# Kernel optimization log

Measured on AMD Instinct MI355X. Metric: run time of the kernel, lower is better.

## Reference

```python
import jax, jax.numpy as jnp
import numpy as np

N = 100000   # nodes
E = 1600000  # edges
F = 128      # n_feat
HID = 64     # n_hid
L = 4        # n_layer
C = 40       # n_class
TEMP = 0.1   # summarize temperature


def setup_inputs() -> dict:
    key = jax.random.key(0)
    ks = jax.random.split(key, 10)
    x = jax.random.normal(ks[0], (N, F), dtype=jnp.float32)
    edge_index = jax.random.randint(ks[1], (2, E), 0, N, dtype=jnp.int64)
    s_in = 1.0 / np.sqrt(F)
    s_h = 1.0 / np.sqrt(HID)
    W0 = jax.random.normal(ks[2], (F, HID), dtype=jnp.float32) * s_in
    b0 = jnp.zeros((HID,), dtype=jnp.float32)
    Ws = jax.random.normal(ks[3], (L - 1, HID, HID), dtype=jnp.float32) * s_h
    bs = jnp.zeros((L - 1, HID), dtype=jnp.float32)
    Wq = jax.random.normal(ks[4], (HID, HID), dtype=jnp.float32) * s_h
    Wk = jax.random.normal(ks[5], (HID, HID), dtype=jnp.float32) * s_h
    Wout = jax.random.normal(ks[6], (HID, C), dtype=jnp.float32) * s_h
    bout = jnp.zeros((C,), dtype=jnp.float32)
    return {"x": x, "edge_index": edge_index, "W0": W0, "b0": b0,
            "Ws": Ws, "bs": bs, "Wq": Wq, "Wk": Wk, "Wout": Wout, "bout": bout}


def reference(x, edge_index, W0, b0, Ws, bs, Wq, Wk, Wout, bout):
    # --- GCN normalization with self-loops (symmetric D^-1/2 (A+I) D^-1/2) ---
    loop = jnp.arange(N, dtype=edge_index.dtype)
    src = jnp.concatenate([edge_index[0], loop])  # [E+N]
    dst = jnp.concatenate([edge_index[1], loop])
    deg = jax.ops.segment_sum(jnp.ones_like(dst, dtype=x.dtype), dst, num_segments=N)
    dinv = jnp.where(deg > 0, jax.lax.rsqrt(deg), 0.0)
    enorm = dinv[src] * dinv[dst]  # [E+N]

    def propagate(h):
        # gather -> scale -> scatter-add (sparse matvec)
        msg = h[src] * enorm[:, None]
        return jax.ops.segment_sum(msg, dst, num_segments=N)

    # --- twin-branch stacked GCN convs (x_ starts as detached copy; eval mode => no dropout) ---
    h, h_ = x, x
    hs, hs_ = [], []
    for l in range(L):
        W = W0 if l == 0 else Ws[l - 1]
        b = b0 if l == 0 else bs[l - 1]
        h = jax.nn.relu(propagate(h @ W) + b)
        h_ = jax.nn.relu(propagate(h_ @ W) + b)
        hs.append(h)
        hs_.append(h_)

    Hm = jnp.stack(hs)    # [L, N, HID]
    Hm_ = jnp.stack(hs_)  # [L, N, HID]

    # --- Summarize: per-node attention over layer scales; query from twin branch ---
    q = jnp.einsum('lnd,de->lne', Hm_, Wq)
    k = jnp.einsum('lnd,de->lne', Hm, Wk)
    scores = jnp.sum(q * k, axis=-1) / TEMP      # [L, N]
    att = jax.nn.softmax(scores, axis=0)         # softmax over layers
    hsum = jnp.einsum('ln,lnd->nd', att, Hm)     # [N, HID]

    return hsum @ Wout + bout                    # [N, C]
```

## Files before the change

### kernel.cpp

```cpp
#include <hip/hip_runtime.h>
#include <hip/hip_bf16.h>
#include <math.h>

#define NN 100000
#define EE 1600000
#define FF 128
#define HH 64
#define CC 40

constexpr int SCAN_B = 1024;
constexpr int NB = (NN + SCAN_B - 1) / SCAN_B;

typedef unsigned long long u64;
typedef float f32x4 __attribute__((ext_vector_type(4)));

constexpr int NBUK = 125;
constexpr int RNB = 800;
constexpr int BCAP3 = 13800;
constexpr int NE_BLK = 4000;
constexpr int ABLK = EE / NE_BLK;

__global__ void k_init(int* __restrict__ bcnt) {
    int i = threadIdx.x;
    if (i < NBUK) bcnt[i] = 0;
}

__global__ __launch_bounds__(256) void k_bucket(const int* __restrict__ ei, int* __restrict__ bcnt,
                                                u64* __restrict__ bpr) {
    __shared__ int lcnt[NBUK], lbase[NBUK], loff[NBUK];
    const int t = threadIdx.x;
    for (int k = t; k < NBUK; k += 256) { lcnt[k] = 0; loff[k] = 0; }
    __syncthreads();
    const int e0 = blockIdx.x * NE_BLK;
    int es[16], ed[16];
#pragma unroll
    for (int k = 0; k < 16; ++k) {
        int idx = t + k * 256;
        if (idx < NE_BLK) {
            es[k] = ei[e0 + idx];
            ed[k] = ei[EE + e0 + idx];
            atomicAdd(&lcnt[ed[k] / RNB], 1);
        }
    }
    __syncthreads();
    for (int k = t; k < NBUK; k += 256) lbase[k] = atomicAdd(&bcnt[k], lcnt[k]);
    __syncthreads();
#pragma unroll
    for (int k = 0; k < 16; ++k) {
        int idx = t + k * 256;
        if (idx < NE_BLK) {
            int b = ed[k] / RNB;
            int pos = lbase[b] + atomicAdd(&loff[b], 1);
            if (pos < BCAP3) {
                bpr[(size_t)b * BCAP3 + pos] = (u64)(unsigned)es[k] | ((u64)(unsigned)ed[k] << 32);
            }
        }
    }
}

__global__ __launch_bounds__(512) void k_count3(const u64* __restrict__ bpr, const int* __restrict__ bcnt,
                                                int* __restrict__ deg) {
    __shared__ int h[RNB];
    const int t = threadIdx.x, b = blockIdx.x;
    for (int k = t; k < RNB; k += 512) h[k] = 0;
    __syncthreads();
    const int cnt = min(bcnt[b], BCAP3);
    const u64* __restrict__ pp = bpr + (size_t)b * BCAP3;
    const int lo = b * RNB;
    for (int i = t; i < cnt; i += 512) atomicAdd(&h[(int)(pp[i] >> 32) - lo], 1);
    __syncthreads();
    for (int k = t; k < RNB; k += 512) deg[lo + k] = h[k] + 1;
}

__global__ void k_dinv(const int* __restrict__ deg, float* __restrict__ dinv) {
    int i = blockIdx.x * 256 + threadIdx.x;
    if (i < NN) dinv[i] = rsqrtf((float)deg[i]);
}

__global__ void k_scanA(const int* __restrict__ deg, int* __restrict__ excl, int* __restrict__ bsum) {
    __shared__ int s[SCAN_B];
    int t = threadIdx.x;
    int g = blockIdx.x * SCAN_B + t;
    int v = (g < NN) ? deg[g] : 0;
    s[t] = v;
    __syncthreads();
    for (int o = 1; o < SCAN_B; o <<= 1) {
        int u = (t >= o) ? s[t - o] : 0;
        __syncthreads();
        s[t] += u;
        __syncthreads();
    }
    if (g < NN) excl[g] = s[t] - v;
    if (t == SCAN_B - 1) bsum[blockIdx.x] = s[t];
}

__global__ void k_scanB(int* __restrict__ bsum) {
    __shared__ int s[128];
    int t = threadIdx.x;
    int v = (t < NB) ? bsum[t] : 0;
    s[t] = v;
    __syncthreads();
    for (int o = 1; o < 128; o <<= 1) {
        int u = (t >= o) ? s[t - o] : 0;
        __syncthreads();
        s[t] += u;
        __syncthreads();
    }
    if (t < NB) bsum[t] = s[t] - v;
}

__global__ void k_scanC(int* __restrict__ rp, const int* __restrict__ bsum) {
    int t = threadIdx.x;
    int g = blockIdx.x * SCAN_B + t;
    if (g < NN) rp[g] = rp[g] + bsum[blockIdx.x];
    if (g == 0) rp[NN] = EE + NN;
}

__global__ __launch_bounds__(512) void k_fill3(const u64* __restrict__ bpr, const int* __restrict__ bcnt,
                                               const int* __restrict__ rp, int* __restrict__ cs) {
    __shared__ int lcur[RNB];
    __shared__ int lbuf[RNB + BCAP3];
    const int t = threadIdx.x, b = blockIdx.x;
    const int lo = b * RNB;
    const int rpl = rp[lo];
    for (int k = t; k < RNB; k += 512) lcur[k] = rp[lo + k] - rpl;
    __syncthreads();
    const int cnt = min(bcnt[b], BCAP3);
    const u64* __restrict__ pp = bpr + (size_t)b * BCAP3;
    for (int i = t; i < cnt; i += 512) {
        u64 u = pp[i];
        int pos = atomicAdd(&lcur[(int)(u >> 32) - lo], 1);
        lbuf[pos] = (int)(unsigned)u;
    }
    __syncthreads();
    for (int k = t; k < RNB; k += 512) {
        int pos = atomicAdd(&lcur[k], 1);
        lbuf[pos] = lo + k;
    }
    __syncthreads();
    const int total = rp[lo + RNB] - rpl;
    for (int i = t; i < total; i += 512) __builtin_nontemporal_store(lbuf[i], cs + rpl + i);
}

template <int K>
__global__ __launch_bounds__(256) void k_gemm(const float* __restrict__ A, const float* __restrict__ W,
                                              const float* __restrict__ dinv, float* __restrict__ Z,
                                              int nrows) {
    constexpr int S = 68;
    __shared__ float wl[64 * 64];
    __shared__ float hl[64 * S];
    const int t = threadIdx.x;
    const int r0 = blockIdx.x * 64;
    const int rg = t >> 4, cg = t & 15;
    float acc[4][4] = {};

    for (int kb = 0; kb < K; kb += 64) {
        {
            const float4* Wv = (const float4*)(W + kb * 64);
            for (int i = t; i < 1024; i += 256) ((float4*)wl)[i] = Wv[i];
        }
        for (int i = t; i < 1024; i += 256) {
            int row = i >> 4, d4 = i & 15;
            float4 v = {0.f, 0.f, 0.f, 0.f};
            if (r0 + row < nrows) v = *(const float4*)(A + (size_t)(r0 + row) * K + kb + d4 * 4);
            *(float4*)(hl + row * S + d4 * 4) = v;
        }
        __syncthreads();
#pragma unroll 8
        for (int d = 0; d < 64; ++d) {
            float4 w4 = *(const float4*)(wl + d * 64 + cg * 4);
#pragma unroll
            for (int i = 0; i < 4; i++) {
                float h = hl[(rg * 4 + i) * S + d];
                acc[i][0] = fmaf(h, w4.x, acc[i][0]);
                acc[i][1] = fmaf(h, w4.y, acc[i][1]);
                acc[i][2] = fmaf(h, w4.z, acc[i][2]);
                acc[i][3] = fmaf(h, w4.w, acc[i][3]);
            }
        }
        __syncthreads();
    }
#pragma unroll
    for (int i = 0; i < 4; i++) {
        int row = r0 + rg * 4 + i;
        if (row < nrows) {
            float dv = dinv[row];
            float4 o = {acc[i][0] * dv, acc[i][1] * dv, acc[i][2] * dv, acc[i][3] * dv};
            *(float4*)(Z + (size_t)row * 64 + cg * 4) = o;
        }
    }
}

__global__ __launch_bounds__(256) void k_prepM(const float* __restrict__ Wq, const float* __restrict__ Wk,
                                               float* __restrict__ M) {
    __shared__ float wk[64 * 65];
    __shared__ float wq[4 * 64];
    const int t = threadIdx.x;
    for (int i = t; i < 1024; i += 256) {
        int r = i >> 4, c4 = i & 15;
        float4 v = ((const float4*)Wk)[i];
        wk[r * 65 + c4 * 4 + 0] = v.x;
        wk[r * 65 + c4 * 4 + 1] = v.y;
        wk[r * 65 + c4 * 4 + 2] = v.z;
        wk[r * 65 + c4 * 4 + 3] = v.w;
    }
    const int rbase = blockIdx.x * 4;
    wq[t] = Wq[rbase * 64 + t];
    __syncthreads();
    const int rr = t >> 6;
    const int c = t & 63;
    float acc = 0.f;
#pragma unroll 8
    for (int e = 0; e < 64; ++e) acc = fmaf(wq[rr * 64 + e], wk[c * 65 + e], acc);
    M[(rbase + rr) * 64 + c] = acc;
}

__global__ __launch_bounds__(256) void k_prop(const float* __restrict__ z, const int* __restrict__ rp,
                                              const int* __restrict__ cs, const float* __restrict__ dinv,
                                              const float* __restrict__ bias, float* __restrict__ out) {
    const int lane = threadIdx.x & 63;
    const int g = lane >> 4;
    const int l4 = lane & 15;
    const int n = blockIdx.x * 16 + (threadIdx.x >> 6) * 4 + g;
    const int beg = rp[n], end = rp[n + 1];
    float4 a0 = {0, 0, 0, 0}, a1 = {0, 0, 0, 0}, a2 = {0, 0, 0, 0}, a3 = {0, 0, 0, 0};
    int i = beg;
    for (; i + 8 <= end; i += 8) {
        int c0 = __builtin_nontemporal_load(cs + i);
        int c1 = __builtin_nontemporal_load(cs + i + 1);
        int c2 = __builtin_nontemporal_load(cs + i + 2);
        int c3 = __builtin_nontemporal_load(cs + i + 3);
        int c4 = __builtin_nontemporal_load(cs + i + 4);
        int c5 = __builtin_nontemporal_load(cs + i + 5);
        int c6 = __builtin_nontemporal_load(cs + i + 6);
        int c7 = __builtin_nontemporal_load(cs + i + 7);
        float4 z0 = *(const float4*)(z + (size_t)(unsigned)c0 * 64 + l4 * 4);
        float4 z1 = *(const float4*)(z + (size_t)(unsigned)c1 * 64 + l4 * 4);
        float4 z2 = *(const float4*)(z + (size_t)(unsigned)c2 * 64 + l4 * 4);
        float4 z3 = *(const float4*)(z + (size_t)(unsigned)c3 * 64 + l4 * 4);
        float4 z4 = *(const float4*)(z + (size_t)(unsigned)c4 * 64 + l4 * 4);
        float4 z5 = *(const float4*)(z + (size_t)(unsigned)c5 * 64 + l4 * 4);
        float4 z6 = *(const float4*)(z + (size_t)(unsigned)c6 * 64 + l4 * 4);
        float4 z7 = *(const float4*)(z + (size_t)(unsigned)c7 * 64 + l4 * 4);
        a0.x += z0.x; a0.y += z0.y; a0.z += z0.z; a0.w += z0.w;
        a1.x += z1.x; a1.y += z1.y; a1.z += z1.z; a1.w += z1.w;
        a2.x += z2.x; a2.y += z2.y; a2.z += z2.z; a2.w += z2.w;
        a3.x += z3.x; a3.y += z3.y; a3.z += z3.z; a3.w += z3.w;
        a0.x += z4.x; a0.y += z4.y; a0.z += z4.z; a0.w += z4.w;
        a1.x += z5.x; a1.y += z5.y; a1.z += z5.z; a1.w += z5.w;
        a2.x += z6.x; a2.y += z6.y; a2.z += z6.z; a2.w += z6.w;
        a3.x += z7.x; a3.y += z7.y; a3.z += z7.z; a3.w += z7.w;
    }
    for (; i + 4 <= end; i += 4) {
        int c0 = __builtin_nontemporal_load(cs + i);
        int c1 = __builtin_nontemporal_load(cs + i + 1);
        int c2 = __builtin_nontemporal_load(cs + i + 2);
        int c3 = __builtin_nontemporal_load(cs + i + 3);
        float4 z0 = *(const float4*)(z + (size_t)(unsigned)c0 * 64 + l4 * 4);
        float4 z1 = *(const float4*)(z + (size_t)(unsigned)c1 * 64 + l4 * 4);
        float4 z2 = *(const float4*)(z + (size_t)(unsigned)c2 * 64 + l4 * 4);
        float4 z3 = *(const float4*)(z + (size_t)(unsigned)c3 * 64 + l4 * 4);
        a0.x += z0.x; a0.y += z0.y; a0.z += z0.z; a0.w += z0.w;
        a1.x += z1.x; a1.y += z1.y; a1.z += z1.z; a1.w += z1.w;
        a2.x += z2.x; a2.y += z2.y; a2.z += z2.z; a2.w += z2.w;
        a3.x += z3.x; a3.y += z3.y; a3.z += z3.z; a3.w += z3.w;
    }
    for (; i < end; ++i) {
        int c = __builtin_nontemporal_load(cs + i);
        float4 zr = *(const float4*)(z + (size_t)(unsigned)c * 64 + l4 * 4);
        a0.x += zr.x; a0.y += zr.y; a0.z += zr.z; a0.w += zr.w;
    }
    const float dn = dinv[n];
    const float4 b4 = *(const float4*)(bias + l4 * 4);
    float4 r;
    r.x = fmaf(dn, (a0.x + a1.x) + (a2.x + a3.x), b4.x);
    r.y = fmaf(dn, (a0.y + a1.y) + (a2.y + a3.y), b4.y);
    r.z = fmaf(dn, (a0.z + a1.z) + (a2.z + a3.z), b4.z);
    r.w = fmaf(dn, (a0.w + a1.w) + (a2.w + a3.w), b4.w);
    r.x = r.x > 0.f ? r.x : 0.f;
    r.y = r.y > 0.f ? r.y : 0.f;
    r.z = r.z > 0.f ? r.z : 0.f;
    r.w = r.w > 0.f ? r.w : 0.f;
    __builtin_nontemporal_store(*(const f32x4*)&r, (f32x4*)(out + (size_t)n * 64 + l4 * 4));
}

__global__ __launch_bounds__(256) void k_scoresum(const float* __restrict__ Hm, const float* __restrict__ Mm,
                                                  const float* __restrict__ Wout, const float* __restrict__ bout,
                                                  float* __restrict__ out) {
    __shared__ float wl[4096];
    __shared__ float hl[64 * 68];
    __shared__ float wo[64 * CC];
    __shared__ float sc[4][64];
    __shared__ float wl4[4][64];
    const int t = threadIdx.x;
    const int r0 = blockIdx.x * 64;
    for (int i = t; i < 1024; i += 256) ((float4*)wl)[i] = ((const float4*)Mm)[i];
    for (int i = t; i < (64 * CC) / 4; i += 256) ((float4*)wo)[i] = ((const float4*)Wout)[i];
    const int rg = t >> 4, cg = t & 15;
    for (int l = 0; l < 4; ++l) {
        __syncthreads();
        for (int i = t; i < 1024; i += 256) {
            int row = i >> 4, d4 = i & 15;
            int n = r0 + row;
            float4 v = {0.f, 0.f, 0.f, 0.f};
            if (n < NN) v = *(const float4*)(Hm + ((size_t)l * NN + n) * 64 + d4 * 4);
            *(float4*)(hl + row * 68 + d4 * 4) = v;
        }
        __syncthreads();
        float u[4][4] = {};
#pragma unroll 8
        for (int d = 0; d < 64; ++d) {
            float4 m4 = *(const float4*)(wl + d * 64 + cg * 4);
#pragma unroll
            for (int i = 0; i < 4; i++) {
                float h = hl[(rg * 4 + i) * 68 + d];
                u[i][0] = fmaf(h, m4.x, u[i][0]);
                u[i][1] = fmaf(h, m4.y, u[i][1]);
                u[i][2] = fmaf(h, m4.z, u[i][2]);
                u[i][3] = fmaf(h, m4.w, u[i][3]);
            }
        }
#pragma unroll
        for (int i = 0; i < 4; i++) {
            const float* hrow = hl + (rg * 4 + i) * 68 + cg * 4;
            float p = u[i][0] * hrow[0] + u[i][1] * hrow[1] + u[i][2] * hrow[2] + u[i][3] * hrow[3];
            p += __shfl_xor(p, 1);
            p += __shfl_xor(p, 2);
            p += __shfl_xor(p, 4);
            p += __shfl_xor(p, 8);
            if (cg == 0) sc[l][rg * 4 + i] = p;
        }
    }
    __syncthreads();
    if (t < 64) {
        float s0 = sc[0][t] * 10.f, s1 = sc[1][t] * 10.f, s2 = sc[2][t] * 10.f, s3 = sc[3][t] * 10.f;
        float m = fmaxf(fmaxf(s0, s1), fmaxf(s2, s3));
        float e0 = __expf(s0 - m), e1 = __expf(s1 - m), e2 = __expf(s2 - m), e3 = __expf(s3 - m);
        float inv = 1.f / (e0 + e1 + e2 + e3);
        wl4[0][t] = e0 * inv;
        wl4[1][t] = e1 * inv;
        wl4[2][t] = e2 * inv;
        wl4[3][t] = e3 * inv;
    }
    __syncthreads();
    for (int i = t; i < 1024; i += 256) {
        int row = i >> 4, d4 = i & 15;
        int n = r0 + row;
        float4 acc = {0.f, 0.f, 0.f, 0.f};
        if (n < NN) {
#pragma unroll
            for (int l = 0; l < 4; ++l) {
                float w = wl4[l][row];
                float4 h = *(const float4*)(Hm + ((size_t)l * NN + n) * 64 + d4 * 4);
                acc.x = fmaf(w, h.x, acc.x);
                acc.y = fmaf(w, h.y, acc.y);
                acc.z = fmaf(w, h.z, acc.z);
                acc.w = fmaf(w, h.w, acc.w);
            }
        }
        *(float4*)(hl + row * 68 + d4 * 4) = acc;
    }
    __syncthreads();
    const int row2 = t >> 2, cg2 = t & 3;
    float2 acc2[5] = {};
    for (int d = 0; d < 64; ++d) {
        float a = hl[row2 * 68 + d];
        const float2* wrow = (const float2*)(wo + d * CC + cg2 * 10);
#pragma unroll
        for (int j = 0; j < 5; ++j) {
            float2 w = wrow[j];
            acc2[j].x = fmaf(a, w.x, acc2[j].x);
            acc2[j].y = fmaf(a, w.y, acc2[j].y);
        }
    }
    int n = r0 + row2;
    if (n < NN) {
        float* op = out + (size_t)n * CC + cg2 * 10;
        const float* bp = bout + cg2 * 10;
#pragma unroll
        for (int j = 0; j < 5; ++j) {
            float2 b = *(const float2*)(bp + 2 * j);
            float2 o = {acc2[j].x + b.x, acc2[j].y + b.y};
            *(float2*)(op + 2 * j) = o;
        }
    }
}

extern "C" void kernel_launch(void* const* d_in, const int* in_sizes, int n_in,
                              void* d_out, int out_size, void* d_ws, size_t ws_size,
                              hipStream_t stream) {
    const float* x    = (const float*)d_in[0];
    const int*   ei   = (const int*)d_in[1];
    const float* W0   = (const float*)d_in[2];
    const float* b0   = (const float*)d_in[3];
    const float* Ws   = (const float*)d_in[4];
    const float* bs   = (const float*)d_in[5];
    const float* Wq   = (const float*)d_in[6];
    const float* Wk   = (const float*)d_in[7];
    const float* Wout = (const float*)d_in[8];
    const float* bout = (const float*)d_in[9];
    float* out = (float*)d_out;

    char* p = (char*)d_ws;
    auto carve = [&](size_t bytes) {
        void* r = (void*)p;
        p += (bytes + 255) & ~(size_t)255;
        return r;
    };
    int*   deg     = (int*)carve((size_t)NN * 4);
    float* dinv    = (float*)carve((size_t)NN * 4);
    int*   row_ptr = (int*)carve((size_t)(NN + 1) * 4);
    int*   bsum    = (int*)carve(256 * 4);
    int*   bcnt    = (int*)carve(NBUK * 4);
    u64*   bpr     = (u64*)carve((size_t)NBUK * BCAP3 * 8);
    int*   cs      = (int*)carve((size_t)(EE + NN) * 4);
    float* M       = (float*)carve((size_t)HH * HH * 4);
    float* z       = (float*)carve((size_t)NN * HH * 4);
    float* Hm      = (float*)carve((size_t)4 * NN * HH * 4);
    (void)ws_size; (void)n_in; (void)in_sizes; (void)out_size;

    const int GB_N = (NN + 255) / 256;
    const int GT   = (NN + 63) / 64;
    const int GP   = NN / 16;
    const int GSS  = (NN + 63) / 64;

    k_init<<<1, 128, 0, stream>>>(bcnt);
    k_bucket<<<ABLK, 256, 0, stream>>>(ei, bcnt, bpr);
    k_count3<<<NBUK, 512, 0, stream>>>(bpr, bcnt, deg);
    k_dinv<<<GB_N, 256, 0, stream>>>(deg, dinv);
    k_scanA<<<NB, SCAN_B, 0, stream>>>(deg, row_ptr, bsum);
    k_scanB<<<1, 128, 0, stream>>>(bsum);
    k_scanC<<<NB, SCAN_B, 0, stream>>>(row_ptr, bsum);
    k_fill3<<<NBUK, 512, 0, stream>>>(bpr, bcnt, row_ptr, cs);
    k_prepM<<<16, 256, 0, stream>>>(Wq, Wk, M);

    k_gemm<FF><<<GT, 256, 0, stream>>>(x, W0, dinv, z, NN);
    k_prop<<<GP, 256, 0, stream>>>(z, row_ptr, cs, dinv, b0, Hm);
    for (int l = 1; l < 4; ++l) {
        k_gemm<HH><<<GT, 256, 0, stream>>>(Hm + (size_t)(l - 1) * NN * HH,
                                           Ws + (size_t)(l - 1) * HH * HH, dinv, z, NN);
        k_prop<<<GP, 256, 0, stream>>>(z, row_ptr, cs, dinv, bs + (size_t)(l - 1) * HH,
                                       Hm + (size_t)l * NN * HH);
    }

    k_scoresum<<<GSS, 256, 0, stream>>>(Hm, M, Wout, bout, out);
}
```

Measured before the change: 594.0 us.

## Stage all four layer tiles in shared memory once in score-sum kernel

The final attention/summary kernel now loads all four layers' 32-row tiles of Hm into shared memory up front, then reuses them for both the score computation and the weighted sum. The old version read Hm from global memory a second time. Blocks shrink to 32 rows with 512 threads, one row per 16-thread group, and the bounds checks are dropped because NN is divisible by 32. Only 128 of the 512 threads do the final output projection, which leaves lanes idle in that phase.

```diff
diff --git a/kernel.cpp b/kernel.cpp
--- a/kernel.cpp
+++ b/kernel.cpp
@@ -284,55 +284,47 @@
     __builtin_nontemporal_store(*(const f32x4*)&r, (f32x4*)(out + (size_t)n * 64 + l4 * 4));
 }
 
-__global__ __launch_bounds__(256) void k_scoresum(const float* __restrict__ Hm, const float* __restrict__ Mm,
+__global__ __launch_bounds__(512) void k_scoresum(const float* __restrict__ Hm, const float* __restrict__ Mm,
                                                   const float* __restrict__ Wout, const float* __restrict__ bout,
                                                   float* __restrict__ out) {
+    __shared__ float hl4[4][32][68];
     __shared__ float wl[4096];
-    __shared__ float hl[64 * 68];
     __shared__ float wo[64 * CC];
-    __shared__ float sc[4][64];
-    __shared__ float wl4[4][64];
+    __shared__ float sc[4][32];
+    __shared__ float wl4[4][32];
     const int t = threadIdx.x;
-    const int r0 = blockIdx.x * 64;
-    for (int i = t; i < 1024; i += 256) ((float4*)wl)[i] = ((const float4*)Mm)[i];
-    for (int i = t; i < (64 * CC) / 4; i += 256) ((float4*)wo)[i] = ((const float4*)Wout)[i];
+    const int r0 = blockIdx.x * 32;
+    for (int i = t; i < 1024; i += 512) ((float4*)wl)[i] = ((const float4*)Mm)[i];
+    for (int i = t; i < (64 * CC) / 4; i += 512) ((float4*)wo)[i] = ((const float4*)Wout)[i];
+    for (int i = t; i < 2048; i += 512) {
+        int l = i >> 9, r = (i >> 4) & 31, d4 = i & 15;
+        float4 v = *(const float4*)(Hm + ((size_t)l * NN + r0 + r) * 64 + d4 * 4);
+        *(float4*)(&hl4[l][r][d4 * 4]) = v;
+    }
+    __syncthreads();
     const int rg = t >> 4, cg = t & 15;
+#pragma unroll
     for (int l = 0; l < 4; ++l) {
-        __syncthreads();
-        for (int i = t; i < 1024; i += 256) {
-            int row = i >> 4, d4 = i & 15;
-            int n = r0 + row;
-            float4 v = {0.f, 0.f, 0.f, 0.f};
-            if (n < NN) v = *(const float4*)(Hm + ((size_t)l * NN + n) * 64 + d4 * 4);
-            *(float4*)(hl + row * 68 + d4 * 4) = v;
-        }
-        __syncthreads();
-        float u[4][4] = {};
+        float u0 = 0.f, u1 = 0.f, u2 = 0.f, u3 = 0.f;
 #pragma unroll 8
         for (int d = 0; d < 64; ++d) {
+            float h = hl4[l][rg][d];
             float4 m4 = *(const float4*)(wl + d * 64 + cg * 4);
-#pragma unroll
-            for (int i = 0; i < 4; i++) {
-                float h = hl[(rg * 4 + i) * 68 + d];
-                u[i][0] = fmaf(h, m4.x, u[i][0]);
-                u[i][1] = fmaf(h, m4.y, u[i][1]);
-                u[i][2] = fmaf(h, m4.z, u[i][2]);
-                u[i][3] = fmaf(h, m4.w, u[i][3]);
-            }
-        }
-#pragma unroll
-        for (int i = 0; i < 4; i++) {
-            const float* hrow = hl + (rg * 4 + i) * 68 + cg * 4;
-            float p = u[i][0] * hrow[0] + u[i][1] * hrow[1] + u[i][2] * hrow[2] + u[i][3] * hrow[3];
-            p += __shfl_xor(p, 1);
-            p += __shfl_xor(p, 2);
-            p += __shfl_xor(p, 4);
-            p += __shfl_xor(p, 8);
-            if (cg == 0) sc[l][rg * 4 + i] = p;
-        }
-    }
-    __syncthreads();
-    if (t < 64) {
+            u0 = fmaf(h, m4.x, u0);
+            u1 = fmaf(h, m4.y, u1);
+            u2 = fmaf(h, m4.z, u2);
+            u3 = fmaf(h, m4.w, u3);
+        }
+        const float* hrow = &hl4[l][rg][cg * 4];
+        float p = u0 * hrow[0] + u1 * hrow[1] + u2 * hrow[2] + u3 * hrow[3];
+        p += __shfl_xor(p, 1);
+        p += __shfl_xor(p, 2);
+        p += __shfl_xor(p, 4);
+        p += __shfl_xor(p, 8);
+        if (cg == 0) sc[l][rg] = p;
+    }
+    __syncthreads();
+    if (t < 32) {
         float s0 = sc[0][t] * 10.f, s1 = sc[1][t] * 10.f, s2 = sc[2][t] * 10.f, s3 = sc[3][t] * 10.f;
         float m = fmaxf(fmaxf(s0, s1), fmaxf(s2, s3));
         float e0 = __expf(s0 - m), e1 = __expf(s1 - m), e2 = __expf(s2 - m), e3 = __expf(s3 - m);
@@ -343,38 +335,35 @@
         wl4[3][t] = e3 * inv;
     }
     __syncthreads();
-    for (int i = t; i < 1024; i += 256) {
-        int row = i >> 4, d4 = i & 15;
-        int n = r0 + row;
-        float4 acc = {0.f, 0.f, 0.f, 0.f};
-        if (n < NN) {
-#pragma unroll
-            for (int l = 0; l < 4; ++l) {
-                float w = wl4[l][row];
-                float4 h = *(const float4*)(Hm + ((size_t)l * NN + n) * 64 + d4 * 4);
-                acc.x = fmaf(w, h.x, acc.x);
-                acc.y = fmaf(w, h.y, acc.y);
-                acc.z = fmaf(w, h.z, acc.z);
-                acc.w = fmaf(w, h.w, acc.w);
+    {
+        int row = t >> 4, d4 = t & 15;
+        float4 h0 = *(const float4*)(&hl4[0][row][d4 * 4]);
+        float4 h1 = *(const float4*)(&hl4[1][row][d4 * 4]);
+        float4 h2 = *(const float4*)(&hl4[2][row][d4 * 4]);
+        float4 h3 = *(const float4*)(&hl4[3][row][d4 * 4]);
+        float w0 = wl4[0][row], w1 = wl4[1][row], w2 = wl4[2][row], w3 = wl4[3][row];
+        float4 acc;
+        acc.x = w0 * h0.x + w1 * h1.x + w2 * h2.x + w3 * h3.x;
+        acc.y = w0 * h0.y + w1 * h1.y + w2 * h2.y + w3 * h3.y;
+        acc.z = w0 * h0.z + w1 * h1.z + w2 * h2.z + w3 * h3.z;
+        acc.w = w0 * h0.w + w1 * h1.w + w2 * h2.w + w3 * h3.w;
+        *(float4*)(&hl4[0][row][d4 * 4]) = acc;
+    }
+    __syncthreads();
+    if (t < 128) {
+        const int row2 = t >> 2, cg2 = t & 3;
+        float2 acc2[5] = {};
+        for (int d = 0; d < 64; ++d) {
+            float a = hl4[0][row2][d];
+            const float2* wrow = (const float2*)(wo + d * CC + cg2 * 10);
+#pragma unroll
+            for (int j = 0; j < 5; ++j) {
+                float2 w = wrow[j];
+                acc2[j].x = fmaf(a, w.x, acc2[j].x);
+                acc2[j].y = fmaf(a, w.y, acc2[j].y);
             }
         }
-        *(float4*)(hl + row * 68 + d4 * 4) = acc;
-    }
-    __syncthreads();
-    const int row2 = t >> 2, cg2 = t & 3;
-    float2 acc2[5] = {};
-    for (int d = 0; d < 64; ++d) {
-        float a = hl[row2 * 68 + d];
-        const float2* wrow = (const float2*)(wo + d * CC + cg2 * 10);
-#pragma unroll
-        for (int j = 0; j < 5; ++j) {
-            float2 w = wrow[j];
-            acc2[j].x = fmaf(a, w.x, acc2[j].x);
-            acc2[j].y = fmaf(a, w.y, acc2[j].y);
-        }
-    }
-    int n = r0 + row2;
-    if (n < NN) {
+        int n = r0 + row2;
         float* op = out + (size_t)n * CC + cg2 * 10;
         const float* bp = bout + cg2 * 10;
 #pragma unroll
@@ -422,7 +411,7 @@
     const int GB_N = (NN + 255) / 256;
     const int GT   = (NN + 63) / 64;
     const int GP   = NN / 16;
-    const int GSS  = (NN + 63) / 64;
+    const int GSS  = NN / 32;
 
     k_init<<<1, 128, 0, stream>>>(bcnt);
     k_bucket<<<ABLK, 256, 0, stream>>>(ei, bcnt, bpr);
@@ -443,5 +432,5 @@
                                        Hm + (size_t)l * NN * HH);
     }
 
-    k_scoresum<<<GSS, 256, 0, stream>>>(Hm, M, Wout, bout, out);
-}
+    k_scoresum<<<GSS, 512, 0, stream>>>(Hm, M, Wout, bout, out);
+}
```

Measured after the change: 613.7 us. +3.3%, slower.

## Restructure score-sum kernel to one node per thread with register accumulation

Applied to the files above, without the earlier changes.

The attention/summarize kernel changes from a tiled 64-node block with shared-memory staging and cross-lane shuffle reductions to one node per thread. Each thread computes the quadratic-form scores for two layers at a time with 32 float4 register accumulators, then does the softmax, weighted sum and output projection entirely in registers. This removes the per-layer syncthreads and shared-memory staging of H, but greatly raises register pressure and reads each node's rows uncoalesced, since threads stride by 256 bytes, and rereads H several times.

```diff
diff --git a/kernel.cpp b/kernel.cpp
--- a/kernel.cpp
+++ b/kernel.cpp
@@ -284,104 +284,119 @@
     __builtin_nontemporal_store(*(const f32x4*)&r, (f32x4*)(out + (size_t)n * 64 + l4 * 4));
 }
 
+template <int L0>
+__device__ __forceinline__ float2 qform2(const float* __restrict__ Hm, const float* __restrict__ wl,
+                                         int nc) {
+    const float* ha = Hm + ((size_t)L0 * NN + nc) * 64;
+    const float* hb = Hm + ((size_t)(L0 + 1) * NN + nc) * 64;
+    float4 ua[16], ub[16];
+#pragma unroll
+    for (int q = 0; q < 16; ++q) {
+        ua[q] = {0.f, 0.f, 0.f, 0.f};
+        ub[q] = {0.f, 0.f, 0.f, 0.f};
+    }
+    for (int dq = 0; dq < 16; ++dq) {
+        float4 h4a = *(const float4*)(ha + dq * 4);
+        float4 h4b = *(const float4*)(hb + dq * 4);
+        const float* m0 = wl + dq * 256;
+#pragma unroll
+        for (int q = 0; q < 16; ++q) {
+            float4 A = *(const float4*)(m0 + q * 4);
+            float4 B = *(const float4*)(m0 + 64 + q * 4);
+            float4 C = *(const float4*)(m0 + 128 + q * 4);
+            float4 D = *(const float4*)(m0 + 192 + q * 4);
+            ua[q].x = fmaf(h4a.x, A.x, ua[q].x); ua[q].y = fmaf(h4a.x, A.y, ua[q].y);
+            ua[q].z = fmaf(h4a.x, A.z, ua[q].z); ua[q].w = fmaf(h4a.x, A.w, ua[q].w);
+            ua[q].x = fmaf(h4a.y, B.x, ua[q].x); ua[q].y = fmaf(h4a.y, B.y, ua[q].y);
+            ua[q].z = fmaf(h4a.y, B.z, ua[q].z); ua[q].w = fmaf(h4a.y, B.w, ua[q].w);
+            ua[q].x = fmaf(h4a.z, C.x, ua[q].x); ua[q].y = fmaf(h4a.z, C.y, ua[q].y);
+            ua[q].z = fmaf(h4a.z, C.z, ua[q].z); ua[q].w = fmaf(h4a.z, C.w, ua[q].w);
+            ua[q].x = fmaf(h4a.w, D.x, ua[q].x); ua[q].y = fmaf(h4a.w, D.y, ua[q].y);
+            ua[q].z = fmaf(h4a.w, D.z, ua[q].z); ua[q].w = fmaf(h4a.w, D.w, ua[q].w);
+            ub[q].x = fmaf(h4b.x, A.x, ub[q].x); ub[q].y = fmaf(h4b.x, A.y, ub[q].y);
+            ub[q].z = fmaf(h4b.x, A.z, ub[q].z); ub[q].w = fmaf(h4b.x, A.w, ub[q].w);
+            ub[q].x = fmaf(h4b.y, B.x, ub[q].x); ub[q].y = fmaf(h4b.y, B.y, ub[q].y);
+            ub[q].z = fmaf(h4b.y, B.z, ub[q].z); ub[q].w = fmaf(h4b.y, B.w, ub[q].w);
+            ub[q].x = fmaf(h4b.z, C.x, ub[q].x); ub[q].y = fmaf(h4b.z, C.y, ub[q].y);
+            ub[q].z = fmaf(h4b.z, C.z, ub[q].z); ub[q].w = fmaf(h4b.z, C.w, ub[q].w);
+            ub[q].x = fmaf(h4b.w, D.x, ub[q].x); ub[q].y = fmaf(h4b.w, D.y, ub[q].y);
+            ub[q].z = fmaf(h4b.w, D.z, ub[q].z); ub[q].w = fmaf(h4b.w, D.w, ub[q].w);
+        }
+    }
+    float sa = 0.f, sb = 0.f;
+#pragma unroll
+    for (int dq = 0; dq < 16; ++dq) {
+        float4 h4a = *(const float4*)(ha + dq * 4);
+        float4 h4b = *(const float4*)(hb + dq * 4);
+        sa += ua[dq].x * h4a.x + ua[dq].y * h4a.y + ua[dq].z * h4a.z + ua[dq].w * h4a.w;
+        sb += ub[dq].x * h4b.x + ub[dq].y * h4b.y + ub[dq].z * h4b.z + ub[dq].w * h4b.w;
+    }
+    return {sa, sb};
+}
+
 __global__ __launch_bounds__(256) void k_scoresum(const float* __restrict__ Hm, const float* __restrict__ Mm,
                                                   const float* __restrict__ Wout, const float* __restrict__ bout,
                                                   float* __restrict__ out) {
     __shared__ float wl[4096];
-    __shared__ float hl[64 * 68];
     __shared__ float wo[64 * CC];
-    __shared__ float sc[4][64];
-    __shared__ float wl4[4][64];
     const int t = threadIdx.x;
-    const int r0 = blockIdx.x * 64;
     for (int i = t; i < 1024; i += 256) ((float4*)wl)[i] = ((const float4*)Mm)[i];
-    for (int i = t; i < (64 * CC) / 4; i += 256) ((float4*)wo)[i] = ((const float4*)Wout)[i];
-    const int rg = t >> 4, cg = t & 15;
-    for (int l = 0; l < 4; ++l) {
-        __syncthreads();
-        for (int i = t; i < 1024; i += 256) {
-            int row = i >> 4, d4 = i & 15;
-            int n = r0 + row;
-            float4 v = {0.f, 0.f, 0.f, 0.f};
-            if (n < NN) v = *(const float4*)(Hm + ((size_t)l * NN + n) * 64 + d4 * 4);
-            *(float4*)(hl + row * 68 + d4 * 4) = v;
-        }
-        __syncthreads();
-        float u[4][4] = {};
-#pragma unroll 8
-        for (int d = 0; d < 64; ++d) {
-            float4 m4 = *(const float4*)(wl + d * 64 + cg * 4);
-#pragma unroll
-            for (int i = 0; i < 4; i++) {
-                float h = hl[(rg * 4 + i) * 68 + d];
-                u[i][0] = fmaf(h, m4.x, u[i][0]);
-                u[i][1] = fmaf(h, m4.y, u[i][1]);
-                u[i][2] = fmaf(h, m4.z, u[i][2]);
-                u[i][3] = fmaf(h, m4.w, u[i][3]);
+    for (int i = t; i < 640; i += 256) ((float4*)wo)[i] = ((const float4*)Wout)[i];
+    __syncthreads();
+    const int n = blockIdx.x * 256 + t;
+    const int nc = n < NN ? n : NN - 1;
+
+    float2 s01 = qform2<0>(Hm, wl, nc);
+    float2 s23 = qform2<2>(Hm, wl, nc);
+
+    float s0 = s01.x * 10.f, s1 = s01.y * 10.f, s2 = s23.x * 10.f, s3 = s23.y * 10.f;
+    float m = fmaxf(fmaxf(s0, s1), fmaxf(s2, s3));
+    float e0 = __expf(s0 - m), e1 = __expf(s1 - m), e2 = __expf(s2 - m), e3 = __expf(s3 - m);
+    float inv = 1.f / (e0 + e1 + e2 + e3);
+    float w0 = e0 * inv, w1 = e1 * inv, w2 = e2 * inv, w3 = e3 * inv;
+
+    const float* h0p = Hm + ((size_t)0 * NN + nc) * 64;
+    const float* h1p = Hm + ((size_t)1 * NN + nc) * 64;
+    const float* h2p = Hm + ((size_t)2 * NN + nc) * 64;
+    const float* h3p = Hm + ((size_t)3 * NN + nc) * 64;
+    float4 hs[16];
+#pragma unroll
+    for (int dq = 0; dq < 16; ++dq) {
+        float4 a = *(const float4*)(h0p + dq * 4);
+        float4 b = *(const float4*)(h1p + dq * 4);
+        float4 c = *(const float4*)(h2p + dq * 4);
+        float4 d = *(const float4*)(h3p + dq * 4);
+        hs[dq].x = w0 * a.x + w1 * b.x + w2 * c.x + w3 * d.x;
+        hs[dq].y = w0 * a.y + w1 * b.y + w2 * c.y + w3 * d.y;
+        hs[dq].z = w0 * a.z + w1 * b.z + w2 * c.z + w3 * d.z;
+        hs[dq].w = w0 * a.w + w1 * b.w + w2 * c.w + w3 * d.w;
+    }
+    float4 acc[10];
+#pragma unroll
+    for (int j = 0; j < 10; ++j) acc[j] = {0.f, 0.f, 0.f, 0.f};
+#pragma unroll
+    for (int dq = 0; dq < 16; ++dq) {
+#pragma unroll
+        for (int r = 0; r < 4; ++r) {
+            float hd = r == 0 ? hs[dq].x : (r == 1 ? hs[dq].y : (r == 2 ? hs[dq].z : hs[dq].w));
+            const float* wrow = wo + (dq * 4 + r) * CC;
+#pragma unroll
+            for (int j = 0; j < 10; ++j) {
+                float4 w = *(const float4*)(wrow + j * 4);
+                acc[j].x = fmaf(hd, w.x, acc[j].x);
+                acc[j].y = fmaf(hd, w.y, acc[j].y);
+                acc[j].z = fmaf(hd, w.z, acc[j].z);
+                acc[j].w = fmaf(hd, w.w, acc[j].w);
             }
         }
-#pragma unroll
-        for (int i = 0; i < 4; i++) {
-            const float* hrow = hl + (rg * 4 + i) * 68 + cg * 4;
-            float p = u[i][0] * hrow[0] + u[i][1] * hrow[1] + u[i][2] * hrow[2] + u[i][3] * hrow[3];
-            p += __shfl_xor(p, 1);
-            p += __shfl_xor(p, 2);
-            p += __shfl_xor(p, 4);
-            p += __shfl_xor(p, 8);
-            if (cg == 0) sc[l][rg * 4 + i] = p;
-        }
-    }
-    __syncthreads();
-    if (t < 64) {
-        float s0 = sc[0][t] * 10.f, s1 = sc[1][t] * 10.f, s2 = sc[2][t] * 10.f, s3 = sc[3][t] * 10.f;
-        float m = fmaxf(fmaxf(s0, s1), fmaxf(s2, s3));
-        float e0 = __expf(s0 - m), e1 = __expf(s1 - m), e2 = __expf(s2 - m), e3 = __expf(s3 - m);
-        float inv = 1.f / (e0 + e1 + e2 + e3);
-        wl4[0][t] = e0 * inv;
-        wl4[1][t] = e1 * inv;
-        wl4[2][t] = e2 * inv;
-        wl4[3][t] = e3 * inv;
-    }
-    __syncthreads();
-    for (int i = t; i < 1024; i += 256) {
-        int row = i >> 4, d4 = i & 15;
-        int n = r0 + row;
-        float4 acc = {0.f, 0.f, 0.f, 0.f};
-        if (n < NN) {
-#pragma unroll
-            for (int l = 0; l < 4; ++l) {
-                float w = wl4[l][row];
-                float4 h = *(const float4*)(Hm + ((size_t)l * NN + n) * 64 + d4 * 4);
-                acc.x = fmaf(w, h.x, acc.x);
-                acc.y = fmaf(w, h.y, acc.y);
-                acc.z = fmaf(w, h.z, acc.z);
-                acc.w = fmaf(w, h.w, acc.w);
-            }
-        }
-        *(float4*)(hl + row * 68 + d4 * 4) = acc;
-    }
-    __syncthreads();
-    const int row2 = t >> 2, cg2 = t & 3;
-    float2 acc2[5] = {};
-    for (int d = 0; d < 64; ++d) {
-        float a = hl[row2 * 68 + d];
-        const float2* wrow = (const float2*)(wo + d * CC + cg2 * 10);
-#pragma unroll
-        for (int j = 0; j < 5; ++j) {
-            float2 w = wrow[j];
-            acc2[j].x = fmaf(a, w.x, acc2[j].x);
-            acc2[j].y = fmaf(a, w.y, acc2[j].y);
-        }
-    }
-    int n = r0 + row2;
+    }
     if (n < NN) {
-        float* op = out + (size_t)n * CC + cg2 * 10;
-        const float* bp = bout + cg2 * 10;
-#pragma unroll
-        for (int j = 0; j < 5; ++j) {
-            float2 b = *(const float2*)(bp + 2 * j);
-            float2 o = {acc2[j].x + b.x, acc2[j].y + b.y};
-            *(float2*)(op + 2 * j) = o;
+        float* op = out + (size_t)n * CC;
+#pragma unroll
+        for (int j = 0; j < 10; ++j) {
+            float4 b = *(const float4*)(bout + j * 4);
+            float4 o = {acc[j].x + b.x, acc[j].y + b.y, acc[j].z + b.z, acc[j].w + b.w};
+            *(float4*)(op + j * 4) = o;
         }
     }
 }
@@ -422,7 +437,7 @@
     const int GB_N = (NN + 255) / 256;
     const int GT   = (NN + 63) / 64;
     const int GP   = NN / 16;
-    const int GSS  = (NN + 63) / 64;
+    const int GSS  = (NN + 255) / 256;
 
     k_init<<<1, 128, 0, stream>>>(bcnt);
     k_bucket<<<ABLK, 256, 0, stream>>>(ei, bcnt, bpr);
```

After: 627.8 us. +5.7%, slower.
